# Kernel tuning notes

Hardware: AMD Instinct MI355X
Metric: run time of the kernel (lower is better)

## Reference

```python
import jax, jax.numpy as jnp
from jax import lax
import numpy as np

B, C, H, W = 8, 128, 256, 256
K_BANK = 4          # num_kernels
KS = 3              # kernel_size
OC = 128            # out_channels


def setup_inputs() -> dict:
    key = jax.random.key(0)
    k1, k2, k3, k4 = jax.random.split(key, 4)
    x = jax.random.normal(k1, (B, C, H, W), dtype=jnp.float32)
    # nn.Parameter(torch.randn(num_kernels, in_channels, 1, ks, ks))
    kernel_bank = jax.random.normal(k2, (K_BANK, C, 1, KS, KS), dtype=jnp.float32)
    # nn.Linear(in_channels, num_kernels)
    attn_w = jax.random.normal(k3, (K_BANK, C), dtype=jnp.float32) * 0.02
    attn_b = jnp.zeros((K_BANK,), dtype=jnp.float32)
    # nn.Conv2d(in_channels, out_channels, 1)
    pw_w = jax.random.normal(k4, (OC, C, 1, 1), dtype=jnp.float32) * 0.05
    pw_b = jnp.zeros((OC,), dtype=jnp.float32)
    return {"x": x, "kernel_bank": kernel_bank, "attn_w": attn_w,
            "attn_b": attn_b, "pw_w": pw_w, "pw_b": pw_b}


def reference(x, kernel_bank, attn_w, attn_b, pw_w, pw_b):
    b, c, h, w = x.shape
    nk, _, _, ks, _ = kernel_bank.shape
    pad = ks // 2
    # GAP -> FC -> softmax attention over kernel bank
    pooled = jnp.mean(x, axis=(2, 3))                          # [B, C]
    attn = jax.nn.softmax(pooled @ attn_w.T + attn_b, axis=1)  # [B, K]
    # per-sample dynamic depthwise kernel: [B, C, ks, ks]
    dyn_kernel = jnp.einsum('bk,kcij->bcij', attn, kernel_bank[:, :, 0])
    # per-sample depthwise conv via grouped conv with B*C groups
    xr = x.reshape(1, b * c, h, w)
    wr = dyn_kernel.reshape(b * c, 1, ks, ks)
    dw = lax.conv_general_dilated(
        xr, wr, window_strides=(1, 1), padding=[(pad, pad), (pad, pad)],
        feature_group_count=b * c,
        dimension_numbers=('NCHW', 'OIHW', 'NCHW'))
    dw = dw.reshape(b, c, h, w)
    # fixed pointwise 1x1 conv
    out = jnp.einsum('bchw,oc->bohw', dw, pw_w[:, :, 0, 0]) + pw_b[None, :, None, None]
    return out
```

## Files before the change

### kernel.cpp

```cpp
#include <hip/hip_runtime.h>
#include <hip/hip_bf16.h>
#include <math.h>

typedef __attribute__((ext_vector_type(8))) short short8;
typedef __attribute__((ext_vector_type(4))) float f32x4;

#define C_IN 128
#define OC_ 128
#define BB 8
#define KBANK 4

__device__ __forceinline__ unsigned short f2bf(float f) {
  union { float f; unsigned int u; } v; v.f = f;
  unsigned int u = v.u;
  unsigned int r = u + 0x7fffu + ((u >> 16) & 1u);
  return (unsigned short)(r >> 16);
}

__global__ void k_pool(const float* __restrict__ x, float* __restrict__ pooled) {
  int plane = blockIdx.x;
  const float4* p = (const float4*)(x + (size_t)plane * 65536);
  float s = 0.f;
  for (int i = threadIdx.x; i < 16384; i += 256) {
    float4 v = p[i];
    s += (v.x + v.y) + (v.z + v.w);
  }
  #pragma unroll
  for (int off = 32; off > 0; off >>= 1) s += __shfl_down(s, off);
  __shared__ float red[4];
  if ((threadIdx.x & 63) == 0) red[threadIdx.x >> 6] = s;
  __syncthreads();
  if (threadIdx.x == 0)
    pooled[plane] = (red[0] + red[1] + red[2] + red[3]) * (1.0f / 65536.0f);
}

__global__ void k_prep(const float* __restrict__ pooled,
                       const float* __restrict__ attn_w,
                       const float* __restrict__ attn_b,
                       const float* __restrict__ bank,
                       const float* __restrict__ pw_w,
                       float* __restrict__ dynk,
                       unsigned short* __restrict__ pwb)
{
  __shared__ float attn_s[BB][KBANK];
  int tid = threadIdx.x;
  if (tid < BB * KBANK) {
    int b = tid >> 2, k = tid & 3;
    float s = attn_b[k];
    for (int c = 0; c < C_IN; ++c) s += pooled[b * C_IN + c] * attn_w[k * C_IN + c];
    attn_s[b][k] = s;
  }
  __syncthreads();
  if (tid < BB) {
    int b = tid;
    float l0 = attn_s[b][0], l1 = attn_s[b][1], l2 = attn_s[b][2], l3 = attn_s[b][3];
    float m = fmaxf(fmaxf(l0, l1), fmaxf(l2, l3));
    float e0 = expf(l0 - m), e1 = expf(l1 - m), e2 = expf(l2 - m), e3 = expf(l3 - m);
    float inv = 1.0f / (e0 + e1 + e2 + e3);
    attn_s[b][0] = e0 * inv; attn_s[b][1] = e1 * inv;
    attn_s[b][2] = e2 * inv; attn_s[b][3] = e3 * inv;
  }
  __syncthreads();
  for (int i = tid; i < BB * C_IN * 9; i += 256) {
    int b = i / (C_IN * 9);
    int rem = i - b * (C_IN * 9);
    float v = 0.f;
    #pragma unroll
    for (int k = 0; k < KBANK; ++k) v += attn_s[b][k] * bank[k * (C_IN * 9) + rem];
    dynk[i] = v;
  }
  for (int i = tid; i < OC_ * C_IN; i += 256) pwb[i] = f2bf(pw_w[i]);
}

__global__ __launch_bounds__(256, 2) void k_main(
    const float* __restrict__ x,
    const float* __restrict__ dynk,
    const unsigned short* __restrict__ pwb,
    const float* __restrict__ pw_b,
    float* __restrict__ out) {
  constexpr int RS = 20;
  constexpr int PS = 10 * RS;
  __shared__ float xs[32 * PS];
  __shared__ unsigned short dws[128 * 40];

  const int b  = blockIdx.z;
  const int h0 = blockIdx.y * 8;
  const int w0 = blockIdx.x * 16;
  const int tid  = threadIdx.x;
  const int wv   = tid >> 6;
  const int lane = tid & 63;
  const int quad = lane >> 4;
  const int l15  = lane & 15;
  const int cl   = tid & 31;
  const int prow = tid >> 5;

  short8 afrag[2][4];
  #pragma unroll
  for (int mt = 0; mt < 2; ++mt) {
    #pragma unroll
    for (int kc = 0; kc < 4; ++kc) {
      int o = wv * 32 + mt * 16 + l15;
      afrag[mt][kc] = *(const short8*)(pwb + ((size_t)o * C_IN + kc * 32 + quad * 8));
    }
  }

  f32x4 acc[2][8];
  #pragma unroll
  for (int mt = 0; mt < 2; ++mt)
    #pragma unroll
    for (int nt = 0; nt < 8; ++nt)
      acc[mt][nt] = (f32x4){0.f, 0.f, 0.f, 0.f};

  #pragma unroll
  for (int kc = 0; kc < 4; ++kc) {
    __syncthreads();
    const int cbase = kc * 32;
    for (int i = tid; i < 5760; i += 256) {
      int c = i / 180;
      int rem = i - c * 180;
      int r = rem / 18;
      int col = rem - r * 18;
      int gh = h0 - 1 + r, gw = w0 - 1 + col;
      float v = 0.f;
      if ((unsigned)gh < 256u && (unsigned)gw < 256u)
        v = x[(((size_t)(b * C_IN + cbase + c)) << 16) + (gh << 8) + gw];
      xs[c * PS + r * RS + col] = v;
    }
    __syncthreads();
    float k9[9];
    {
      const float* kp = dynk + (size_t)(b * C_IN + cbase + cl) * 9;
      #pragma unroll
      for (int t = 0; t < 9; ++t) k9[t] = kp[t];
    }
    float accd[16];
    #pragma unroll
    for (int col = 0; col < 16; ++col) accd[col] = 0.f;
    const float* xp = &xs[cl * PS + prow * RS];
    #pragma unroll
    for (int i = 0; i < 3; ++i) {
      float xr[18];
      const float* rp = xp + i * RS;
      #pragma unroll
      for (int j = 0; j < 9; ++j) {
        float2 t = *(const float2*)(rp + 2 * j);
        xr[2 * j] = t.x; xr[2 * j + 1] = t.y;
      }
      float c0 = k9[3 * i], c1 = k9[3 * i + 1], c2 = k9[3 * i + 2];
      #pragma unroll
      for (int col = 0; col < 16; ++col)
        accd[col] = fmaf(c0, xr[col], fmaf(c1, xr[col + 1], fmaf(c2, xr[col + 2], accd[col])));
    }
    #pragma unroll
    for (int col = 0; col < 16; ++col)
      dws[(prow * 16 + col) * 40 + cl] = f2bf(accd[col]);
    __syncthreads();
    #pragma unroll
    for (int nt = 0; nt < 8; ++nt) {
      short8 bfrag = *(const short8*)&dws[(nt * 16 + l15) * 40 + quad * 8];
      acc[0][nt] = __builtin_amdgcn_mfma_f32_16x16x32_bf16(afrag[0][kc], bfrag, acc[0][nt], 0, 0, 0);
      acc[1][nt] = __builtin_amdgcn_mfma_f32_16x16x32_bf16(afrag[1][kc], bfrag, acc[1][nt], 0, 0, 0);
    }
  }
  #pragma unroll
  for (int mt = 0; mt < 2; ++mt) {
    #pragma unroll
    for (int r = 0; r < 4; ++r) {
      int o = wv * 32 + mt * 16 + quad * 4 + r;
      float bias = pw_b[o];
      size_t obase = ((size_t)(b * OC_ + o)) << 16;
      #pragma unroll
      for (int nt = 0; nt < 8; ++nt)
        out[obase + ((h0 + nt) << 8) + (w0 + l15)] = acc[mt][nt][r] + bias;
    }
  }
}

extern "C" void kernel_launch(void* const* d_in, const int* in_sizes, int n_in,
                              void* d_out, int out_size, void* d_ws, size_t ws_size,
                              hipStream_t stream) {
  const float* x      = (const float*)d_in[0];
  const float* bank   = (const float*)d_in[1];
  const float* attn_w = (const float*)d_in[2];
  const float* attn_b = (const float*)d_in[3];
  const float* pw_w   = (const float*)d_in[4];
  const float* pw_b   = (const float*)d_in[5];
  float* out = (float*)d_out;

  char* ws = (char*)d_ws;
  float* pooled       = (float*)ws;
  float* dynk         = (float*)(ws + 4096);
  unsigned short* pwb = (unsigned short*)(ws + 4096 + 36864);

  k_pool<<<1024, 256, 0, stream>>>(x, pooled);
  k_prep<<<1, 256, 0, stream>>>(pooled, attn_w, attn_b, bank, pw_w, dynk, pwb);
  dim3 grid(16, 32, 8);
  k_main<<<grid, 256, 0, stream>>>(x, dynk, pwb, pw_b, out);
}
```

Measured before the change: 793.3 us.

## Vectorize halo tile loads, retune LDS padding and occupancy, parallelize pool and FC

The main kernel's halo tile load changes from a scalar loop with divisions to per-thread float4 row loads. Each thread copies one 18-wide row for a fixed channel and row, with precomputed boundary flags. The LDS row stride becomes 18 and the plane stride 181 to cut bank conflicts, but this drops the float2 LDS reads for scalar ones. Launch bounds rise to 3 blocks per CU. The pooling loop is unrolled with four independent accumulators, and the attention FC is split across 8 lanes with shuffle reduction.

```diff
diff --git a/kernel.cpp b/kernel.cpp
--- a/kernel.cpp
+++ b/kernel.cpp
@@ -20,11 +20,18 @@
 __global__ void k_pool(const float* __restrict__ x, float* __restrict__ pooled) {
   int plane = blockIdx.x;
   const float4* p = (const float4*)(x + (size_t)plane * 65536);
-  float s = 0.f;
-  for (int i = threadIdx.x; i < 16384; i += 256) {
-    float4 v = p[i];
-    s += (v.x + v.y) + (v.z + v.w);
-  }
+  float s0 = 0.f, s1 = 0.f, s2 = 0.f, s3 = 0.f;
+  for (int i = threadIdx.x; i < 16384; i += 1024) {
+    float4 a = p[i];
+    float4 b = p[i + 256];
+    float4 c = p[i + 512];
+    float4 d = p[i + 768];
+    s0 += (a.x + a.y) + (a.z + a.w);
+    s1 += (b.x + b.y) + (b.z + b.w);
+    s2 += (c.x + c.y) + (c.z + c.w);
+    s3 += (d.x + d.y) + (d.z + d.w);
+  }
+  float s = (s0 + s1) + (s2 + s3);
   #pragma unroll
   for (int off = 32; off > 0; off >>= 1) s += __shfl_down(s, off);
   __shared__ float red[4];
@@ -44,11 +51,19 @@
 {
   __shared__ float attn_s[BB][KBANK];
   int tid = threadIdx.x;
-  if (tid < BB * KBANK) {
-    int b = tid >> 2, k = tid & 3;
-    float s = attn_b[k];
-    for (int c = 0; c < C_IN; ++c) s += pooled[b * C_IN + c] * attn_w[k * C_IN + c];
-    attn_s[b][k] = s;
+  {
+    int pr = tid >> 3, g = tid & 7;
+    int b = pr >> 2, k = pr & 3;
+    float s = 0.f;
+    #pragma unroll
+    for (int j = 0; j < 16; ++j) {
+      int c = g * 16 + j;
+      s += pooled[b * C_IN + c] * attn_w[k * C_IN + c];
+    }
+    s += __shfl_xor(s, 1);
+    s += __shfl_xor(s, 2);
+    s += __shfl_xor(s, 4);
+    if (g == 0) attn_s[b][k] = s + attn_b[k];
   }
   __syncthreads();
   if (tid < BB) {
@@ -72,14 +87,14 @@
   for (int i = tid; i < OC_ * C_IN; i += 256) pwb[i] = f2bf(pw_w[i]);
 }
 
-__global__ __launch_bounds__(256, 2) void k_main(
+__global__ __launch_bounds__(256, 3) void k_main(
     const float* __restrict__ x,
     const float* __restrict__ dynk,
     const unsigned short* __restrict__ pwb,
     const float* __restrict__ pw_b,
     float* __restrict__ out) {
-  constexpr int RS = 20;
-  constexpr int PS = 10 * RS;
+  constexpr int RS = 18;
+  constexpr int PS = 181;
   __shared__ float xs[32 * PS];
   __shared__ unsigned short dws[128 * 40];
 
@@ -94,15 +109,29 @@
   const int cl   = tid & 31;
   const int prow = tid >> 5;
 
+  const int c0 = tid >> 3, r0 = tid & 7;
+  const int gh0 = h0 - 1 + r0;
+  const bool ok0 = (unsigned)gh0 < 256u;
+  const float* g0 = x + (((size_t)(b * C_IN + c0)) << 16)
+                      + (size_t)(ok0 ? gh0 : 0) * 256 + (w0 - 1);
+  float* s0p = xs + c0 * PS + r0 * RS;
+  const int c1 = tid >> 1, r1 = 8 + (tid & 1);
+  const int gh1 = h0 - 1 + r1;
+  const bool ok1 = (unsigned)gh1 < 256u;
+  const float* g1 = x + (((size_t)(b * C_IN + c1)) << 16)
+                      + (size_t)(ok1 ? gh1 : 0) * 256 + (w0 - 1);
+  float* s1p = xs + c1 * PS + r1 * RS;
+  const bool has2 = tid < 64;
+  const bool wL = (w0 > 0), wR = (w0 < 240);
+
   short8 afrag[2][4];
   #pragma unroll
-  for (int mt = 0; mt < 2; ++mt) {
+  for (int mt = 0; mt < 2; ++mt)
     #pragma unroll
     for (int kc = 0; kc < 4; ++kc) {
       int o = wv * 32 + mt * 16 + l15;
       afrag[mt][kc] = *(const short8*)(pwb + ((size_t)o * C_IN + kc * 32 + quad * 8));
     }
-  }
 
   f32x4 acc[2][8];
   #pragma unroll
@@ -114,22 +143,52 @@
   #pragma unroll
   for (int kc = 0; kc < 4; ++kc) {
     __syncthreads();
-    const int cbase = kc * 32;
-    for (int i = tid; i < 5760; i += 256) {
-      int c = i / 180;
-      int rem = i - c * 180;
-      int r = rem / 18;
-      int col = rem - r * 18;
-      int gh = h0 - 1 + r, gw = w0 - 1 + col;
-      float v = 0.f;
-      if ((unsigned)gh < 256u && (unsigned)gw < 256u)
-        v = x[(((size_t)(b * C_IN + cbase + c)) << 16) + (gh << 8) + gw];
-      xs[c * PS + r * RS + col] = v;
+    {
+      float v[18];
+      if (ok0) {
+        float4 a = *(const float4*)(g0 + 1);
+        float4 bq = *(const float4*)(g0 + 5);
+        float4 cq = *(const float4*)(g0 + 9);
+        float4 dq = *(const float4*)(g0 + 13);
+        v[0] = wL ? g0[0] : 0.f;
+        v[17] = wR ? g0[17] : 0.f;
+        v[1] = a.x; v[2] = a.y; v[3] = a.z; v[4] = a.w;
+        v[5] = bq.x; v[6] = bq.y; v[7] = bq.z; v[8] = bq.w;
+        v[9] = cq.x; v[10] = cq.y; v[11] = cq.z; v[12] = cq.w;
+        v[13] = dq.x; v[14] = dq.y; v[15] = dq.z; v[16] = dq.w;
+      } else {
+        #pragma unroll
+        for (int j = 0; j < 18; ++j) v[j] = 0.f;
+      }
+      #pragma unroll
+      for (int j = 0; j < 18; ++j) s0p[j] = v[j];
+      if (has2) {
+        float u[18];
+        if (ok1) {
+          float4 a = *(const float4*)(g1 + 1);
+          float4 bq = *(const float4*)(g1 + 5);
+          float4 cq = *(const float4*)(g1 + 9);
+          float4 dq = *(const float4*)(g1 + 13);
+          u[0] = wL ? g1[0] : 0.f;
+          u[17] = wR ? g1[17] : 0.f;
+          u[1] = a.x; u[2] = a.y; u[3] = a.z; u[4] = a.w;
+          u[5] = bq.x; u[6] = bq.y; u[7] = bq.z; u[8] = bq.w;
+          u[9] = cq.x; u[10] = cq.y; u[11] = cq.z; u[12] = cq.w;
+          u[13] = dq.x; u[14] = dq.y; u[15] = dq.z; u[16] = dq.w;
+        } else {
+          #pragma unroll
+          for (int j = 0; j < 18; ++j) u[j] = 0.f;
+        }
+        #pragma unroll
+        for (int j = 0; j < 18; ++j) s1p[j] = u[j];
+      }
+      g0 += (size_t)32 << 16;
+      g1 += (size_t)32 << 16;
     }
     __syncthreads();
     float k9[9];
     {
-      const float* kp = dynk + (size_t)(b * C_IN + cbase + cl) * 9;
+      const float* kp = dynk + (size_t)(b * C_IN + kc * 32 + cl) * 9;
       #pragma unroll
       for (int t = 0; t < 9; ++t) k9[t] = kp[t];
     }
@@ -142,14 +201,11 @@
       float xr[18];
       const float* rp = xp + i * RS;
       #pragma unroll
-      for (int j = 0; j < 9; ++j) {
-        float2 t = *(const float2*)(rp + 2 * j);
-        xr[2 * j] = t.x; xr[2 * j + 1] = t.y;
-      }
-      float c0 = k9[3 * i], c1 = k9[3 * i + 1], c2 = k9[3 * i + 2];
+      for (int j = 0; j < 18; ++j) xr[j] = rp[j];
+      float cc0 = k9[3 * i], cc1 = k9[3 * i + 1], cc2 = k9[3 * i + 2];
       #pragma unroll
       for (int col = 0; col < 16; ++col)
-        accd[col] = fmaf(c0, xr[col], fmaf(c1, xr[col + 1], fmaf(c2, xr[col + 2], accd[col])));
+        accd[col] = fmaf(cc0, xr[col], fmaf(cc1, xr[col + 1], fmaf(cc2, xr[col + 2], accd[col])));
     }
     #pragma unroll
     for (int col = 0; col < 16; ++col)
```

Result: faster. 637.8 us (-19.6%).
